# Kernel tuning notes

Measured on AMD Instinct MI355X. Metric: run time of the kernel, lower is better.

## Reference

```python
import jax, jax.numpy as jnp
import numpy as np

STRIDE = 8.0
N_CLS = 80


def setup_inputs() -> dict:
    key = jax.random.key(0)
    k1, k2, k3 = jax.random.split(key, 3)
    nB, nH, nW = 16, 128, 128
    bbox = jax.random.normal(k1, (nB, nH, nW, 4), dtype=jnp.float32)
    center = jax.random.normal(k2, (nB, nH, nW, 1), dtype=jnp.float32)
    cls_logits = jax.random.normal(k3, (nB, nH, nW, N_CLS), dtype=jnp.float32)
    return {"bbox": bbox, "center": center, "cls_logits": cls_logits}


def _ltrb_to_xywh(ltrb, stride):
    # ltrb: [nB, nH, nW, 4] with (left, top, right, bottom) distances
    nH, nW = ltrb.shape[1], ltrb.shape[2]
    cy = (jnp.arange(nH, dtype=ltrb.dtype) * stride + stride / 2)[None, :, None]
    cx = (jnp.arange(nW, dtype=ltrb.dtype) * stride + stride / 2)[None, None, :]
    l, t, r, b = ltrb[..., 0], ltrb[..., 1], ltrb[..., 2], ltrb[..., 3]
    x = cx - (l - r) / 2
    y = cy - (t - b) / 2
    w = l + r
    h = t + b
    return jnp.stack([x, y, w, h], axis=-1)


def reference(bbox, center, cls_logits):
    nB = bbox.shape[0]
    # ltrb_setting = 'exp_sl1' -> exp branch of inference decode
    p_ltrb = jnp.exp(bbox) * STRIDE                      # [nB,nH,nW,4]
    p_xywh = _ltrb_to_xywh(p_ltrb, STRIDE)               # [nB,nH,nW,4]
    p_center_conf = jax.nn.sigmoid(center)               # [nB,nH,nW,1]
    p_cls = jax.nn.sigmoid(cls_logits)                   # [nB,nH,nW,C]
    cls_score = jnp.max(p_cls, axis=3, keepdims=True)    # [nB,nH,nW,1]
    cls_idx = jnp.argmax(p_cls, axis=3)                  # [nB,nH,nW]
    confs = jnp.sqrt(p_center_conf * cls_score)          # [nB,nH,nW,1]
    return (p_xywh.reshape(nB, -1, 4),
            cls_idx.reshape(nB, -1),
            confs.reshape(nB, -1))
```

## Files before the change

### kernel.cpp

```cpp
#include <hip/hip_runtime.h>
#include <math.h>

#define NB   16
#define NH   128
#define NW   128
#define NCLS 80
#define NPOS (NB * NH * NW)
#define STRIDE_F 8.0f

__global__ __launch_bounds__(256) void fcos_decode_kernel(
    const float* __restrict__ bbox,
    const float* __restrict__ center,
    const float* __restrict__ cls,
    float* __restrict__ out)
{
    const int pos = blockIdx.x * blockDim.x + threadIdx.x;
    if (pos >= NPOS) return;

    const int w = pos & (NW - 1);
    const int h = (pos >> 7) & (NH - 1);

    const float4 ltrb = *(const float4*)(bbox + (size_t)pos * 4);
    const float l = expf(ltrb.x) * STRIDE_F;
    const float t = expf(ltrb.y) * STRIDE_F;
    const float r = expf(ltrb.z) * STRIDE_F;
    const float b = expf(ltrb.w) * STRIDE_F;

    const float cx = (float)w * STRIDE_F + STRIDE_F * 0.5f;
    const float cy = (float)h * STRIDE_F + STRIDE_F * 0.5f;

    const float x  = cx - (l - r) * 0.5f;
    const float y  = cy - (t - b) * 0.5f;
    const float bw = l + r;
    const float bh = t + b;

    const float4* cp = (const float4*)(cls + (size_t)pos * NCLS);
    float best = -INFINITY;
    int   bidx = 0;
    #pragma unroll
    for (int j = 0; j < NCLS / 4; ++j) {
        const float4 v = cp[j];
        const int c = j * 4;
        if (v.x > best) { best = v.x; bidx = c;     }
        if (v.y > best) { best = v.y; bidx = c + 1; }
        if (v.z > best) { best = v.z; bidx = c + 2; }
        if (v.w > best) { best = v.w; bidx = c + 3; }
    }
    const float cls_score = 1.0f / (1.0f + expf(-best));

    const float cen = 1.0f / (1.0f + expf(-center[pos]));
    const float conf = sqrtf(cen * cls_score);

    ((float4*)out)[pos] = make_float4(x, y, bw, bh);
    out[(size_t)4 * NPOS + pos] = (float)bidx;
    out[(size_t)5 * NPOS + pos] = conf;
}

extern "C" void kernel_launch(void* const* d_in, const int* in_sizes, int n_in,
                              void* d_out, int out_size, void* d_ws, size_t ws_size,
                              hipStream_t stream)
{
    const float* bbox   = (const float*)d_in[0];
    const float* center = (const float*)d_in[1];
    const float* cls    = (const float*)d_in[2];
    float* out = (float*)d_out;

    const int threads = 256;
    const int blocks  = (NPOS + threads - 1) / threads;
    fcos_decode_kernel<<<blocks, threads, 0, stream>>>(bbox, center, cls, out);
}
```

Measured before the change: 134.2 us.

## Split bbox decode and class argmax into separate block ranges with 4 lanes per position

The kernel is split by block index. One range of blocks decodes boxes one position per thread. The other range handles the class argmax with four lanes per position, each scanning 20 classes and then reducing with xor shuffles that break ties toward the lower index. Before, each thread read 320 strided bytes on its own, so the cls loads were poorly coalesced; now neighbouring lanes read contiguous 80-byte chunks and the load spreads across four times as many threads. In exchange there are more blocks, only one lane in four does the stores, and the shuffle reduction costs a few extra instructions.

```diff
diff --git a/kernel.cpp b/kernel.cpp
--- a/kernel.cpp
+++ b/kernel.cpp
@@ -8,52 +8,75 @@
 #define NPOS (NB * NH * NW)
 #define STRIDE_F 8.0f
 
+#define BLOCKS_A (NPOS / 256)
+#define BLOCKS_B (NPOS / 64)
+
 __global__ __launch_bounds__(256) void fcos_decode_kernel(
     const float* __restrict__ bbox,
     const float* __restrict__ center,
     const float* __restrict__ cls,
     float* __restrict__ out)
 {
-    const int pos = blockIdx.x * blockDim.x + threadIdx.x;
-    if (pos >= NPOS) return;
+    const int bid = blockIdx.x;
 
-    const int w = pos & (NW - 1);
-    const int h = (pos >> 7) & (NH - 1);
+    if (bid < BLOCKS_A) {
+        const int pos = bid * 256 + threadIdx.x;
+        const int w = pos & (NW - 1);
+        const int h = (pos >> 7) & (NH - 1);
 
-    const float4 ltrb = *(const float4*)(bbox + (size_t)pos * 4);
-    const float l = expf(ltrb.x) * STRIDE_F;
-    const float t = expf(ltrb.y) * STRIDE_F;
-    const float r = expf(ltrb.z) * STRIDE_F;
-    const float b = expf(ltrb.w) * STRIDE_F;
+        const float4 ltrb = ((const float4*)bbox)[pos];
+        const float l = expf(ltrb.x) * STRIDE_F;
+        const float t = expf(ltrb.y) * STRIDE_F;
+        const float r = expf(ltrb.z) * STRIDE_F;
+        const float b = expf(ltrb.w) * STRIDE_F;
 
-    const float cx = (float)w * STRIDE_F + STRIDE_F * 0.5f;
-    const float cy = (float)h * STRIDE_F + STRIDE_F * 0.5f;
+        const float cx = (float)w * STRIDE_F + STRIDE_F * 0.5f;
+        const float cy = (float)h * STRIDE_F + STRIDE_F * 0.5f;
 
-    const float x  = cx - (l - r) * 0.5f;
-    const float y  = cy - (t - b) * 0.5f;
-    const float bw = l + r;
-    const float bh = t + b;
+        ((float4*)out)[pos] = make_float4(cx - (l - r) * 0.5f,
+                                          cy - (t - b) * 0.5f,
+                                          l + r,
+                                          t + b);
+    } else {
+        const int b    = bid - BLOCKS_A;
+        const int wave = threadIdx.x >> 6;
+        const int lane = threadIdx.x & 63;
+        const int p    = lane >> 2;
+        const int q    = lane & 3;
+        const int pos  = b * 64 + wave * 16 + p;
 
-    const float4* cp = (const float4*)(cls + (size_t)pos * NCLS);
-    float best = -INFINITY;
-    int   bidx = 0;
-    #pragma unroll
-    for (int j = 0; j < NCLS / 4; ++j) {
-        const float4 v = cp[j];
-        const int c = j * 4;
-        if (v.x > best) { best = v.x; bidx = c;     }
-        if (v.y > best) { best = v.y; bidx = c + 1; }
-        if (v.z > best) { best = v.z; bidx = c + 2; }
-        if (v.w > best) { best = v.w; bidx = c + 3; }
+        const float4* cp = (const float4*)(cls + (size_t)pos * NCLS + q * 20);
+        const float4 v0 = cp[0];
+        const float4 v1 = cp[1];
+        const float4 v2 = cp[2];
+        const float4 v3 = cp[3];
+        const float4 v4 = cp[4];
+
+        float best = v0.x; int li = 0;
+        #define SCAN(val, j) if ((val) > best) { best = (val); li = (j); }
+        SCAN(v0.y, 1)  SCAN(v0.z, 2)  SCAN(v0.w, 3)
+        SCAN(v1.x, 4)  SCAN(v1.y, 5)  SCAN(v1.z, 6)  SCAN(v1.w, 7)
+        SCAN(v2.x, 8)  SCAN(v2.y, 9)  SCAN(v2.z, 10) SCAN(v2.w, 11)
+        SCAN(v3.x, 12) SCAN(v3.y, 13) SCAN(v3.z, 14) SCAN(v3.w, 15)
+        SCAN(v4.x, 16) SCAN(v4.y, 17) SCAN(v4.z, 18) SCAN(v4.w, 19)
+        #undef SCAN
+        int idx = q * 20 + li;
+
+        #pragma unroll
+        for (int mask = 1; mask <= 2; mask <<= 1) {
+            const float ov = __shfl_xor(best, mask);
+            const int   oi = __shfl_xor(idx,  mask);
+            if (ov > best || (ov == best && oi < idx)) { best = ov; idx = oi; }
+        }
+
+        if (q == 0) {
+            const float cen  = center[pos];
+            const float sc   = 1.0f / (1.0f + expf(-cen));
+            const float ss   = 1.0f / (1.0f + expf(-best));
+            out[(size_t)4 * NPOS + pos] = (float)idx;
+            out[(size_t)5 * NPOS + pos] = sqrtf(sc * ss);
+        }
     }
-    const float cls_score = 1.0f / (1.0f + expf(-best));
-
-    const float cen = 1.0f / (1.0f + expf(-center[pos]));
-    const float conf = sqrtf(cen * cls_score);
-
-    ((float4*)out)[pos] = make_float4(x, y, bw, bh);
-    out[(size_t)4 * NPOS + pos] = (float)bidx;
-    out[(size_t)5 * NPOS + pos] = conf;
 }
 
 extern "C" void kernel_launch(void* const* d_in, const int* in_sizes, int n_in,
@@ -65,7 +88,5 @@
     const float* cls    = (const float*)d_in[2];
     float* out = (float*)d_out;
 
-    const int threads = 256;
-    const int blocks  = (NPOS + threads - 1) / threads;
-    fcos_decode_kernel<<<blocks, threads, 0, stream>>>(bbox, center, cls, out);
+    fcos_decode_kernel<<<BLOCKS_A + BLOCKS_B, 256, 0, stream>>>(bbox, center, cls, out);
 }
```

New measurement: 126.6 us. 1.06x faster.
